# Performance work log

Measured on AMD Instinct MI355X. Metric: run time of the kernel, lower is better.

Reference implementation:

```python
import jax, jax.numpy as jnp
import numpy as np

ALPHA = 0.01  # ELU slope from init kwargs


def setup_inputs() -> dict:
    key = jax.random.key(0)
    k1, k2, k3, k4, k5 = jax.random.split(key, 5)
    B, L, D_IN, D_ATT = 8, 2048, 256, 128
    context = jax.random.normal(k1, (B, L, D_IN), dtype=jnp.float32)
    query = jax.random.normal(k2, (B, L, D_IN), dtype=jnp.float32)
    query_mask = jax.random.randint(k3, (B, L), 0, 2, dtype=jnp.int32)
    # Linear(in_size, attention_size, bias=False) weights (stored as [in, out])
    W_in = jax.random.normal(k4, (D_IN, D_ATT), dtype=jnp.float32) * 0.05
    W_mem = jax.random.normal(k5, (D_IN, D_ATT), dtype=jnp.float32) * 0.05
    return {"context": context, "query": query, "W_in": W_in,
            "W_mem": W_mem, "query_mask": query_mask}


def reference(context, query, W_in, W_mem, query_mask):
    # VariationalDropout is identity at inference; Linear -> ELU(alpha=0.01)
    inp = jax.nn.elu(jnp.einsum('bld,df->blf', context, W_in), ALPHA)   # [B, Lc, Datt]
    mem = jax.nn.elu(jnp.einsum('bld,df->blf', query, W_mem), ALPHA)    # [B, Lq, Datt]
    scale = inp.shape[-1] ** 0.5
    logits = jnp.einsum('bcf,bqf->bcq', inp, mem) / scale               # [B, Lc, Lq]
    big = jnp.finfo(logits.dtype).max
    # mask_diag=True: kill diagonal (self) positions
    Lq = logits.shape[-1]
    eye = jnp.eye(Lq, dtype=bool)
    logits = jnp.where(eye[None, :, :], -big, logits)
    # masked_softmax over the query axis using query_mask [B, Lq]
    valid = (query_mask > 0)[:, None, :]                                # [B, 1, Lq]
    logits = jnp.where(valid, logits, -big)
    score = jax.nn.softmax(logits, axis=-1)                             # [B, Lc, Lq]
    return jnp.einsum('bcq,bqd->bcd', score, query)                     # [B, Lc, D_in]
```

## Files before the change

kernel.cpp:

```cpp
#include <hip/hip_runtime.h>
#include <math.h>

typedef short v4s __attribute__((ext_vector_type(4)));
typedef short v8s __attribute__((ext_vector_type(8)));
typedef float v4f __attribute__((ext_vector_type(4)));

#define L2E 1.4426950408889634f
#define INV_SCALE 0.08838834764831845f
#define SCL2 (INV_SCALE * L2E)

static __device__ __forceinline__ short f2bf(float x) {
    union { float f; unsigned u; } c; c.f = x;
    unsigned u = c.u;
    unsigned r = (u + 0x7fffu + ((u >> 16) & 1u)) >> 16;
    return (short)r;
}

__global__ __launch_bounds__(256) void k_wt(const float* __restrict__ Win,
                                            const float* __restrict__ Wmem,
                                            short* __restrict__ WtIn,
                                            short* __restrict__ WtMem) {
    const float* W = blockIdx.y ? Wmem : Win;
    short* Wt = blockIdx.y ? WtMem : WtIn;
    int id0 = blockIdx.x * 1024;
#pragma unroll
    for (int i = 0; i < 4; ++i) {
        int id = id0 + i * 256 + threadIdx.x;
        int f = id >> 8, k = id & 255;
        Wt[id] = f2bf(W[k * 128 + f]);
    }
}

__global__ __launch_bounds__(256) void k_main(const float* __restrict__ ctx,
                                              const float* __restrict__ qry,
                                              const short* __restrict__ WtIn,
                                              const short* __restrict__ WtMem,
                                              const int* __restrict__ qmask,
                                              short* __restrict__ Qa,
                                              short* __restrict__ Ka,
                                              short* __restrict__ VaT,
                                              float* __restrict__ maskadd) {
    __shared__ float tile[64][65];
    int x = blockIdx.x;
    int tid = threadIdx.x;
    if (x < 512) {
        int msel = x & 255, isel = x >> 8;
        const float* X = isel ? qry : ctx;
        const short* Wt = isel ? WtMem : WtIn;
        short* Y = isel ? Ka : Qa;
        int w = tid >> 6, lane = tid & 63;
        int ln = lane & 15, qd = lane >> 4;
        int m0 = msel * 64 + w * 16;

        v8s a[8];
#pragma unroll
        for (int kk = 0; kk < 8; ++kk) {
            const float* xp = X + (size_t)(m0 + ln) * 256 + kk * 32 + qd * 8;
            float4 x0 = *(const float4*)xp;
            float4 x1 = *(const float4*)(xp + 4);
            a[kk][0] = f2bf(x0.x); a[kk][1] = f2bf(x0.y);
            a[kk][2] = f2bf(x0.z); a[kk][3] = f2bf(x0.w);
            a[kk][4] = f2bf(x1.x); a[kk][5] = f2bf(x1.y);
            a[kk][6] = f2bf(x1.z); a[kk][7] = f2bf(x1.w);
        }
        v4f zero = {0.f, 0.f, 0.f, 0.f};
        v4f o[8];
#pragma unroll
        for (int i = 0; i < 8; ++i) o[i] = zero;
#pragma unroll
        for (int kk = 0; kk < 8; ++kk)
#pragma unroll
            for (int nt = 0; nt < 8; ++nt) {
                v8s bfr = *(const v8s*)(Wt + (size_t)(nt * 16 + ln) * 256 + kk * 32 + qd * 8);
                o[nt] = __builtin_amdgcn_mfma_f32_16x16x32_bf16(a[kk], bfr, o[nt], 0, 0, 0);
            }
#pragma unroll
        for (int nt = 0; nt < 8; ++nt)
#pragma unroll
            for (int r = 0; r < 4; ++r) {
                float v = o[nt][r];
                v = v > 0.f ? v : 0.01f * (__expf(v) - 1.f);
                Y[(size_t)(m0 + qd * 4 + r) * 128 + nt * 16 + ln] = f2bf(v);
            }
    } else {
        int t = x - 512;
        int q0 = (t & 31) * 64, d0 = ((t >> 5) & 3) * 64, b = t >> 7;
        int c = tid & 63;
        int r4 = tid >> 6;
#pragma unroll
        for (int i = 0; i < 16; ++i) {
            int r = r4 + i * 4;
            tile[r][c] = qry[(size_t)(b * 2048 + q0 + r) * 256 + d0 + c];
        }
        __syncthreads();
#pragma unroll
        for (int i = 0; i < 16; ++i) {
            int d = r4 + i * 4;
            VaT[(size_t)(b * 256 + d0 + d) * 2048 + q0 + c] = f2bf(tile[c][d]);
        }
        if (d0 == 0 && tid < 64) {
            int qq = b * 2048 + q0 + tid;
            maskadd[qq] = (qmask[qq] > 0) ? 0.f : -__builtin_inff();
        }
    }
}

__global__ __launch_bounds__(256, 1) void k_attn(const short* __restrict__ Qa,
                                                 const short* __restrict__ Ka,
                                                 const short* __restrict__ VaT,
                                                 const float* __restrict__ maskadd,
                                                 float* __restrict__ out) {
    __shared__ __align__(16) short PS[2][64 * 72];
    __shared__ float lS[4][64];

    int blk = blockIdx.x;
    int b = blk & 7;
    int c0 = (blk >> 3) * 64;
    int tid = threadIdx.x;
    int w = tid >> 6, lane = tid & 63, ln = lane & 15, qd = lane >> 4;

    v8s qf[4][4];
#pragma unroll
    for (int ct = 0; ct < 4; ++ct) {
        const short* qp = Qa + (size_t)(b * 2048 + c0 + ct * 16 + ln) * 128 + qd * 8;
#pragma unroll
        for (int kk = 0; kk < 4; ++kk) qf[ct][kk] = *(const v8s*)(qp + kk * 32);
    }

    v4f zero = {0.f, 0.f, 0.f, 0.f};
    v4f o[4][4];
#pragma unroll
    for (int i = 0; i < 4; ++i)
#pragma unroll
        for (int j = 0; j < 4; ++j) o[i][j] = zero;
    float lacc[4] = {0.f, 0.f, 0.f, 0.f};

    const short* kbase = Ka + (size_t)(b * 2048 + w * 16 + ln) * 128 + qd * 8;
    const short* vbase = VaT + (size_t)(b * 256) * 2048;
    const float* mbase = maskadd + b * 2048 + w * 16 + qd * 4;

    for (int it = 0; it < 32; ++it) {
        int q0 = it * 64, pb = it & 1;
        v8s kf[4];
        const short* kp = kbase + (size_t)q0 * 128;
#pragma unroll
        for (int kk = 0; kk < 4; ++kk) kf[kk] = *(const v8s*)(kp + kk * 32);
        float4 mk = *(const float4*)(mbase + q0);
        v8s vf[2][4];
#pragma unroll
        for (int kk2 = 0; kk2 < 2; ++kk2)
#pragma unroll
            for (int dt = 0; dt < 4; ++dt)
                vf[kk2][dt] = *(const v8s*)(vbase + (size_t)(w * 64 + dt * 16 + ln) * 2048
                                            + q0 + kk2 * 32 + qd * 8);

        int kvb = q0 + w * 16 + qd * 4;
#pragma unroll
        for (int ct = 0; ct < 4; ++ct) {
            v4f s = zero;
#pragma unroll
            for (int kk = 0; kk < 4; ++kk)
                s = __builtin_amdgcn_mfma_f32_16x16x32_bf16(kf[kk], qf[ct][kk], s, 0, 0, 0);
            int cg = c0 + ct * 16 + ln;
            v4s pw;
            float ls = 0.f;
#pragma unroll
            for (int r = 0; r < 4; ++r) {
                float v = s[r] * SCL2 + (&mk.x)[r];
                if (kvb + r == cg) v = -__builtin_inff();
                float p = exp2f(v);
                ls += p;
                pw[r] = f2bf(p);
            }
            lacc[ct] += ls;
            *(v4s*)(&PS[pb][(ct * 16 + ln) * 72 + w * 16 + qd * 4]) = pw;
        }
        __syncthreads();

#pragma unroll
        for (int kk2 = 0; kk2 < 2; ++kk2) {
            v8s pf[4];
#pragma unroll
            for (int ct = 0; ct < 4; ++ct)
                pf[ct] = *(const v8s*)(&PS[pb][(ct * 16 + ln) * 72 + kk2 * 32 + qd * 8]);
#pragma unroll
            for (int ct = 0; ct < 4; ++ct)
#pragma unroll
                for (int dt = 0; dt < 4; ++dt)
                    o[ct][dt] = __builtin_amdgcn_mfma_f32_16x16x32_bf16(pf[ct], vf[kk2][dt], o[ct][dt], 0, 0, 0);
        }
    }

#pragma unroll
    for (int ct = 0; ct < 4; ++ct) {
        float v = lacc[ct];
        v += __shfl_xor(v, 16);
        v += __shfl_xor(v, 32);
        if (qd == 0) lS[w][ct * 16 + ln] = v;
    }
    __syncthreads();

#pragma unroll
    for (int ct = 0; ct < 4; ++ct) {
        int rowg = b * 2048 + c0 + ct * 16 + qd * 4;
#pragma unroll
        for (int r = 0; r < 4; ++r) {
            int ci = ct * 16 + qd * 4 + r;
            float lv = lS[0][ci] + lS[1][ci] + lS[2][ci] + lS[3][ci];
            float inv = 1.f / lv;
#pragma unroll
            for (int dt = 0; dt < 4; ++dt)
                out[(size_t)(rowg + r) * 256 + w * 64 + dt * 16 + ln] = o[ct][dt][r] * inv;
        }
    }
}

extern "C" void kernel_launch(void* const* d_in, const int* in_sizes, int n_in,
                              void* d_out, int out_size, void* d_ws, size_t ws_size,
                              hipStream_t stream) {
    const float* ctx  = (const float*)d_in[0];
    const float* qry  = (const float*)d_in[1];
    const float* win  = (const float*)d_in[2];
    const float* wmem = (const float*)d_in[3];
    const int* qmask  = (const int*)d_in[4];
    float* out = (float*)d_out;

    char* ws = (char*)d_ws;
    short* Qa      = (short*)(ws);
    short* Ka      = (short*)(ws + (4u << 20));
    short* VaT     = (short*)(ws + (8u << 20));
    float* maskadd = (float*)(ws + (16u << 20));
    short* WtIn    = (short*)(ws + (16u << 20) + 65536);
    short* WtMem   = (short*)(ws + (16u << 20) + 131072);

    k_wt<<<dim3(32, 2), 256, 0, stream>>>(win, wmem, WtIn, WtMem);
    k_main<<<dim3(1536), 256, 0, stream>>>(ctx, qry, WtIn, WtMem, qmask,
                                           Qa, Ka, VaT, maskadd);
    k_attn<<<dim3(256), 256, 0, stream>>>(Qa, Ka, VaT, maskadd, out);
}
```

Baseline: 160.6 us.

## Split attention over KV halves with smaller row tiles and fuse V transpose into projection

The attention kernel now handles 32 context rows per block instead of 64 and can split the key/value range into two halves. Each half writes unnormalized partial outputs and row sums, and a new combine kernel adds them and normalizes. This raises the block count from 256 to 1024 and sets launch bounds for 3 blocks per CU, so the GPU should fill better. The V transpose is also folded into the query projection path by reusing the bf16 registers, and conversions use packed bf16 intrinsics. The cost is extra global traffic for the fp32 partials, an extra launch, less reuse of K/V per block, and strided scalar stores for VaT.

```diff
diff --git a/kernel.cpp b/kernel.cpp
--- a/kernel.cpp
+++ b/kernel.cpp
@@ -1,4 +1,5 @@
 #include <hip/hip_runtime.h>
+#include <hip/hip_bf16.h>
 #include <math.h>
 
 typedef short v4s __attribute__((ext_vector_type(4)));
@@ -14,6 +15,11 @@
     unsigned u = c.u;
     unsigned r = (u + 0x7fffu + ((u >> 16) & 1u)) >> 16;
     return (short)r;
+}
+static __device__ __forceinline__ unsigned pk2(float a, float b) {
+    union { __hip_bfloat162 h; unsigned u; } c;
+    c.h = __float22bfloat162_rn(float2{a, b});
+    return c.u;
 }
 
 __global__ __launch_bounds__(256) void k_wt(const float* __restrict__ Win,
@@ -40,151 +46,149 @@
                                               short* __restrict__ Ka,
                                               short* __restrict__ VaT,
                                               float* __restrict__ maskadd) {
-    __shared__ float tile[64][65];
     int x = blockIdx.x;
+    int isel = x >> 8, msel = x & 255;
+    const float* X = isel ? qry : ctx;
+    const short* Wt = isel ? WtMem : WtIn;
+    short* Y = isel ? Ka : Qa;
     int tid = threadIdx.x;
-    if (x < 512) {
-        int msel = x & 255, isel = x >> 8;
-        const float* X = isel ? qry : ctx;
-        const short* Wt = isel ? WtMem : WtIn;
-        short* Y = isel ? Ka : Qa;
-        int w = tid >> 6, lane = tid & 63;
-        int ln = lane & 15, qd = lane >> 4;
-        int m0 = msel * 64 + w * 16;
-
-        v8s a[8];
-#pragma unroll
-        for (int kk = 0; kk < 8; ++kk) {
-            const float* xp = X + (size_t)(m0 + ln) * 256 + kk * 32 + qd * 8;
-            float4 x0 = *(const float4*)xp;
-            float4 x1 = *(const float4*)(xp + 4);
-            a[kk][0] = f2bf(x0.x); a[kk][1] = f2bf(x0.y);
-            a[kk][2] = f2bf(x0.z); a[kk][3] = f2bf(x0.w);
-            a[kk][4] = f2bf(x1.x); a[kk][5] = f2bf(x1.y);
-            a[kk][6] = f2bf(x1.z); a[kk][7] = f2bf(x1.w);
-        }
-        v4f zero = {0.f, 0.f, 0.f, 0.f};
-        v4f o[8];
-#pragma unroll
-        for (int i = 0; i < 8; ++i) o[i] = zero;
+    int w = tid >> 6, lane = tid & 63, ln = lane & 15, qd = lane >> 4;
+    int m0 = msel * 64 + w * 16;
+
+    v8s a[8];
+#pragma unroll
+    for (int kk = 0; kk < 8; ++kk) {
+        const float* xp = X + (size_t)(m0 + ln) * 256 + kk * 32 + qd * 8;
+        float4 x0 = *(const float4*)xp;
+        float4 x1 = *(const float4*)(xp + 4);
+        unsigned* au = (unsigned*)&a[kk];
+        au[0] = pk2(x0.x, x0.y); au[1] = pk2(x0.z, x0.w);
+        au[2] = pk2(x1.x, x1.y); au[3] = pk2(x1.z, x1.w);
+    }
+    if (isel) {
+        int b = (msel * 64) >> 11, q0 = (msel * 64) & 2047;
+        int qloc = q0 + w * 16 + ln;
 #pragma unroll
         for (int kk = 0; kk < 8; ++kk)
 #pragma unroll
-            for (int nt = 0; nt < 8; ++nt) {
-                v8s bfr = *(const v8s*)(Wt + (size_t)(nt * 16 + ln) * 256 + kk * 32 + qd * 8);
-                o[nt] = __builtin_amdgcn_mfma_f32_16x16x32_bf16(a[kk], bfr, o[nt], 0, 0, 0);
-            }
-#pragma unroll
-        for (int nt = 0; nt < 8; ++nt)
-#pragma unroll
-            for (int r = 0; r < 4; ++r) {
-                float v = o[nt][r];
-                v = v > 0.f ? v : 0.01f * (__expf(v) - 1.f);
-                Y[(size_t)(m0 + qd * 4 + r) * 128 + nt * 16 + ln] = f2bf(v);
-            }
-    } else {
-        int t = x - 512;
-        int q0 = (t & 31) * 64, d0 = ((t >> 5) & 3) * 64, b = t >> 7;
-        int c = tid & 63;
-        int r4 = tid >> 6;
-#pragma unroll
-        for (int i = 0; i < 16; ++i) {
-            int r = r4 + i * 4;
-            tile[r][c] = qry[(size_t)(b * 2048 + q0 + r) * 256 + d0 + c];
-        }
-        __syncthreads();
-#pragma unroll
-        for (int i = 0; i < 16; ++i) {
-            int d = r4 + i * 4;
-            VaT[(size_t)(b * 256 + d0 + d) * 2048 + q0 + c] = f2bf(tile[c][d]);
-        }
-        if (d0 == 0 && tid < 64) {
+            for (int j = 0; j < 8; ++j)
+                VaT[(size_t)(b * 256 + kk * 32 + qd * 8 + j) * 2048 + qloc] = a[kk][j];
+        if (tid < 64) {
             int qq = b * 2048 + q0 + tid;
             maskadd[qq] = (qmask[qq] > 0) ? 0.f : -__builtin_inff();
         }
     }
-}
-
-__global__ __launch_bounds__(256, 1) void k_attn(const short* __restrict__ Qa,
+    v4f zero = {0.f, 0.f, 0.f, 0.f};
+    v4f o[8];
+#pragma unroll
+    for (int i = 0; i < 8; ++i) o[i] = zero;
+#pragma unroll
+    for (int kk = 0; kk < 8; ++kk)
+#pragma unroll
+        for (int nt = 0; nt < 8; ++nt) {
+            v8s bfr = *(const v8s*)(Wt + (size_t)(nt * 16 + ln) * 256 + kk * 32 + qd * 8);
+            o[nt] = __builtin_amdgcn_mfma_f32_16x16x32_bf16(a[kk], bfr, o[nt], 0, 0, 0);
+        }
+#pragma unroll
+    for (int nt = 0; nt < 8; ++nt)
+#pragma unroll
+        for (int r = 0; r < 4; ++r) {
+            float v = o[nt][r];
+            v = v > 0.f ? v : 0.01f * (__expf(v) - 1.f);
+            Y[(size_t)(m0 + qd * 4 + r) * 128 + nt * 16 + ln] = f2bf(v);
+        }
+}
+
+template<int NSPLIT, bool DIRECT>
+__global__ __launch_bounds__(256, 3) void k_attn(const short* __restrict__ Qa,
                                                  const short* __restrict__ Ka,
                                                  const short* __restrict__ VaT,
                                                  const float* __restrict__ maskadd,
+                                                 float* __restrict__ Opart,
+                                                 float* __restrict__ lpart,
                                                  float* __restrict__ out) {
-    __shared__ __align__(16) short PS[2][64 * 72];
-    __shared__ float lS[4][64];
-
+    __shared__ __align__(16) short PS[2][32 * 72];
+    __shared__ float lS[4][32];
+
+    const int STEPS = 32 / NSPLIT;
     int blk = blockIdx.x;
     int b = blk & 7;
-    int c0 = (blk >> 3) * 64;
+    int t = blk >> 3;
+    int c0 = (t & 63) * 32;
+    int sp = t >> 6;
+    int kv0 = sp * (2048 / NSPLIT);
+
     int tid = threadIdx.x;
     int w = tid >> 6, lane = tid & 63, ln = lane & 15, qd = lane >> 4;
 
-    v8s qf[4][4];
-#pragma unroll
-    for (int ct = 0; ct < 4; ++ct) {
+    v8s qf[2][4];
+#pragma unroll
+    for (int ct = 0; ct < 2; ++ct) {
         const short* qp = Qa + (size_t)(b * 2048 + c0 + ct * 16 + ln) * 128 + qd * 8;
 #pragma unroll
         for (int kk = 0; kk < 4; ++kk) qf[ct][kk] = *(const v8s*)(qp + kk * 32);
     }
 
     v4f zero = {0.f, 0.f, 0.f, 0.f};
-    v4f o[4][4];
-#pragma unroll
-    for (int i = 0; i < 4; ++i)
+    v4f o[2][4];
+#pragma unroll
+    for (int i = 0; i < 2; ++i)
 #pragma unroll
         for (int j = 0; j < 4; ++j) o[i][j] = zero;
-    float lacc[4] = {0.f, 0.f, 0.f, 0.f};
-
-    const short* kbase = Ka + (size_t)(b * 2048 + w * 16 + ln) * 128 + qd * 8;
-    const short* vbase = VaT + (size_t)(b * 256) * 2048;
-    const float* mbase = maskadd + b * 2048 + w * 16 + qd * 4;
-
-    for (int it = 0; it < 32; ++it) {
-        int q0 = it * 64, pb = it & 1;
+    float lacc[2] = {0.f, 0.f};
+
+    const short* kbase = Ka + (size_t)(b * 2048 + kv0 + w * 16 + ln) * 128 + qd * 8;
+    const short* vbase = VaT + (size_t)(b * 256) * 2048 + kv0;
+    const float* mbase = maskadd + b * 2048 + kv0 + w * 16 + qd * 4;
+
+    for (int it = 0; it < STEPS; ++it) {
+        int pb = it & 1;
         v8s kf[4];
-        const short* kp = kbase + (size_t)q0 * 128;
+        const short* kp = kbase + (size_t)it * (64 * 128);
 #pragma unroll
         for (int kk = 0; kk < 4; ++kk) kf[kk] = *(const v8s*)(kp + kk * 32);
-        float4 mk = *(const float4*)(mbase + q0);
+        float4 mk = *(const float4*)(mbase + it * 64);
         v8s vf[2][4];
 #pragma unroll
         for (int kk2 = 0; kk2 < 2; ++kk2)
 #pragma unroll
             for (int dt = 0; dt < 4; ++dt)
                 vf[kk2][dt] = *(const v8s*)(vbase + (size_t)(w * 64 + dt * 16 + ln) * 2048
-                                            + q0 + kk2 * 32 + qd * 8);
-
-        int kvb = q0 + w * 16 + qd * 4;
-#pragma unroll
-        for (int ct = 0; ct < 4; ++ct) {
+                                            + it * 64 + kk2 * 32 + qd * 8);
+
+        int kvb = kv0 + it * 64 + w * 16 + qd * 4;
+#pragma unroll
+        for (int ct = 0; ct < 2; ++ct) {
             v4f s = zero;
 #pragma unroll
             for (int kk = 0; kk < 4; ++kk)
                 s = __builtin_amdgcn_mfma_f32_16x16x32_bf16(kf[kk], qf[ct][kk], s, 0, 0, 0);
             int cg = c0 + ct * 16 + ln;
-            v4s pw;
+            float p[4];
             float ls = 0.f;
 #pragma unroll
             for (int r = 0; r < 4; ++r) {
                 float v = s[r] * SCL2 + (&mk.x)[r];
                 if (kvb + r == cg) v = -__builtin_inff();
-                float p = exp2f(v);
-                ls += p;
-                pw[r] = f2bf(p);
+                p[r] = exp2f(v);
+                ls += p[r];
             }
             lacc[ct] += ls;
+            v4s pw;
+            ((unsigned*)&pw)[0] = pk2(p[0], p[1]);
+            ((unsigned*)&pw)[1] = pk2(p[2], p[3]);
             *(v4s*)(&PS[pb][(ct * 16 + ln) * 72 + w * 16 + qd * 4]) = pw;
         }
         __syncthreads();
 
 #pragma unroll
         for (int kk2 = 0; kk2 < 2; ++kk2) {
-            v8s pf[4];
-#pragma unroll
-            for (int ct = 0; ct < 4; ++ct)
+            v8s pf[2];
+#pragma unroll
+            for (int ct = 0; ct < 2; ++ct)
                 pf[ct] = *(const v8s*)(&PS[pb][(ct * 16 + ln) * 72 + kk2 * 32 + qd * 8]);
 #pragma unroll
-            for (int ct = 0; ct < 4; ++ct)
+            for (int ct = 0; ct < 2; ++ct)
 #pragma unroll
                 for (int dt = 0; dt < 4; ++dt)
                     o[ct][dt] = __builtin_amdgcn_mfma_f32_16x16x32_bf16(pf[ct], vf[kk2][dt], o[ct][dt], 0, 0, 0);
@@ -192,7 +196,7 @@
     }
 
 #pragma unroll
-    for (int ct = 0; ct < 4; ++ct) {
+    for (int ct = 0; ct < 2; ++ct) {
         float v = lacc[ct];
         v += __shfl_xor(v, 16);
         v += __shfl_xor(v, 32);
@@ -201,18 +205,47 @@
     __syncthreads();
 
 #pragma unroll
-    for (int ct = 0; ct < 4; ++ct) {
+    for (int ct = 0; ct < 2; ++ct) {
         int rowg = b * 2048 + c0 + ct * 16 + qd * 4;
 #pragma unroll
         for (int r = 0; r < 4; ++r) {
             int ci = ct * 16 + qd * 4 + r;
             float lv = lS[0][ci] + lS[1][ci] + lS[2][ci] + lS[3][ci];
-            float inv = 1.f / lv;
-#pragma unroll
-            for (int dt = 0; dt < 4; ++dt)
-                out[(size_t)(rowg + r) * 256 + w * 64 + dt * 16 + ln] = o[ct][dt][r] * inv;
-        }
-    }
+            if (DIRECT) {
+                float inv = 1.f / lv;
+#pragma unroll
+                for (int dt = 0; dt < 4; ++dt)
+                    out[(size_t)(rowg + r) * 256 + w * 64 + dt * 16 + ln] = o[ct][dt][r] * inv;
+            } else {
+                float* op = Opart + (size_t)sp * (16384 * 256);
+#pragma unroll
+                for (int dt = 0; dt < 4; ++dt)
+                    op[(size_t)(rowg + r) * 256 + w * 64 + dt * 16 + ln] = o[ct][dt][r];
+            }
+        }
+    }
+    if (!DIRECT && tid < 32)
+        lpart[sp * 16384 + b * 2048 + c0 + tid] =
+            lS[0][tid] + lS[1][tid] + lS[2][tid] + lS[3][tid];
+}
+
+template<int NSPLIT>
+__global__ __launch_bounds__(256) void k_combine(const float* __restrict__ Opart,
+                                                 const float* __restrict__ lpart,
+                                                 float* __restrict__ out) {
+    int idx = blockIdx.x * 256 + threadIdx.x;
+    int row = idx >> 6, d4 = (idx & 63) * 4;
+    float L = 0.f;
+    float4 acc = {0.f, 0.f, 0.f, 0.f};
+#pragma unroll
+    for (int s = 0; s < NSPLIT; ++s) {
+        L += lpart[s * 16384 + row];
+        float4 v = *(const float4*)(Opart + (size_t)s * (16384 * 256) + (size_t)row * 256 + d4);
+        acc.x += v.x; acc.y += v.y; acc.z += v.z; acc.w += v.w;
+    }
+    float inv = 1.f / L;
+    float4 res = {acc.x * inv, acc.y * inv, acc.z * inv, acc.w * inv};
+    *(float4*)(out + (size_t)row * 256 + d4) = res;
 }
 
 extern "C" void kernel_launch(void* const* d_in, const int* in_sizes, int n_in,
@@ -232,9 +265,18 @@
     float* maskadd = (float*)(ws + (16u << 20));
     short* WtIn    = (short*)(ws + (16u << 20) + 65536);
     short* WtMem   = (short*)(ws + (16u << 20) + 131072);
+    float* lpart   = (float*)(ws + (16u << 20) + 196608);
+    float* Opart   = (float*)(ws + (18u << 20));
 
     k_wt<<<dim3(32, 2), 256, 0, stream>>>(win, wmem, WtIn, WtMem);
-    k_main<<<dim3(1536), 256, 0, stream>>>(ctx, qry, WtIn, WtMem, qmask,
-                                           Qa, Ka, VaT, maskadd);
-    k_attn<<<dim3(256), 256, 0, stream>>>(Qa, Ka, VaT, maskadd, out);
-}
+    k_main<<<dim3(512), 256, 0, stream>>>(ctx, qry, WtIn, WtMem, qmask,
+                                          Qa, Ka, VaT, maskadd);
+
+    const size_t base = 18u << 20, part = 16u << 20;
+    if (ws_size >= base + 2 * part) {
+        k_attn<2, false><<<dim3(1024), 256, 0, stream>>>(Qa, Ka, VaT, maskadd, Opart, lpart, out);
+        k_combine<2><<<dim3(4096), 256, 0, stream>>>(Opart, lpart, out);
+    } else {
+        k_attn<1, true><<<dim3(512), 256, 0, stream>>>(Qa, Ka, VaT, maskadd, Opart, lpart, out);
+    }
+}
```

After: 205.3 us. 27.8% more time.
